# Performance work log

Hardware: AMD Instinct MI355X
Metric: run time of the kernel (lower is better)

## Reference

```python
import jax, jax.numpy as jnp
import numpy as np

H, W, K = 1024, 2048, 64


def _make_xy_coords(h, w):
    # matches torch buffer: xy_coords[0] = x coords (1..w), xy_coords[1] = y coords (1..h)
    x = jnp.tile(jnp.arange(1, w + 1, dtype=jnp.float32)[None, :], (h, 1))
    y = jnp.tile(jnp.arange(1, h + 1, dtype=jnp.float32)[:, None], (1, w))
    return jnp.stack((x, y), 0)  # (2, H, W)


def setup_inputs() -> dict:
    key = jax.random.key(0)
    k1, k2 = jax.random.split(key)
    instance_regressions = jax.random.normal(k1, (2, H, W), dtype=jnp.float32) * 32.0
    # center_coords[:, 0] = y in [0, H), center_coords[:, 1] = x in [0, W)
    u = jax.random.uniform(k2, (K, 2), dtype=jnp.float32)
    center_coords = u * jnp.array([H, W], dtype=jnp.float32)
    xy_coords = _make_xy_coords(H, W)
    return {
        "instance_regressions": instance_regressions,
        "center_coords": center_coords,
        "xy_coords": xy_coords,
    }


def reference(instance_regressions, center_coords, xy_coords):
    # predicted center for every pixel: (2, H, W)
    pred = xy_coords - instance_regressions
    px, py = pred[0], pred[1]                      # (H, W) each
    cy, cx = center_coords[:, 0], center_coords[:, 1]  # (k,) each; note column order
    dx = px[:, :, None] - cx[None, None, :]        # (H, W, k)
    dy = py[:, :, None] - cy[None, None, :]        # (H, W, k)
    dist = jnp.sqrt(dx * dx + dy * dy)             # (H, W, k)
    closest_inds = jnp.argmin(dist, axis=-1) + 1   # (H, W) int, 1-based instance ids
    return closest_inds
```

## Files before the change

### kernel.cpp

```cpp
#include <hip/hip_runtime.h>


#define H_ 1024
#define W_ 2048
#define K_ 64
#define TAU 8.0f

__global__ __launch_bounds__(256) void inst_map_kernel(
    const float* __restrict__ reg,
    const float* __restrict__ cc,
    int* __restrict__ out)
{
    __shared__ float4 cand[4][K_ + 1];

    const int tid  = threadIdx.x;
    const int w    = tid >> 6;
    const int lane = tid & 63;
    const int tr0  = blockIdx.y * 32;
    const int tc0  = blockIdx.x * 32;
    const int r    = tr0 + w * 8 + (lane >> 3);
    const int c    = tc0 + ((lane & 7) << 2);
    const int base = r * W_ + c;

    const float4 rx = *reinterpret_cast<const float4*>(reg + base);
    const float4 ry = *reinterpret_cast<const float4*>(reg + H_ * W_ + base);

    const float ax = (float)tc0 + 16.5f;
    const float ay = (float)(tr0 + w * 8) + 4.5f;

    float px[4], py[4];
    const float yf = (float)(r + 1);
    px[0] = (float)(c + 1) - rx.x;  py[0] = yf - ry.x;
    px[1] = (float)(c + 2) - rx.y;  py[1] = yf - ry.y;
    px[2] = (float)(c + 3) - rx.z;  py[2] = yf - ry.z;
    px[3] = (float)(c + 4) - rx.w;  py[3] = yf - ry.w;

    float pxn[4], pyn[4];
    float m = 0.0f;
    #pragma unroll
    for (int i = 0; i < 4; ++i) {
        const float sx = px[i] - ax, sy = py[i] - ay;
        pxn[i] = -2.0f * sx;
        pyn[i] = -2.0f * sy;
        m = fmaxf(m, sx * sx + sy * sy);
    }
    #pragma unroll
    for (int s = 1; s < 64; s <<= 1)
        m = fmaxf(m, __shfl_xor(m, s, 64));
    const float Rt = sqrtf(m);

    const float cyk = cc[2 * lane];
    const float cxk = cc[2 * lane + 1];
    const float sx = cxk - ax, sy = cyk - ay;
    const float ck = sx * sx + sy * sy;
    const float d  = sqrtf(ck);
    float dmin = d;
    #pragma unroll
    for (int s = 1; s < 64; s <<= 1)
        dmin = fminf(dmin, __shfl_xor(dmin, s, 64));
    const bool keep = d <= dmin + 2.0f * Rt + 4.0f;
    const unsigned long long mask = __ballot(keep);
    const int ncand = (int)__popcll(mask);
    if (keep) {
        const int pos = (int)__popcll(mask & ((1ull << lane) - 1ull));
        cand[w][pos] = make_float4(sx, sy, ck, __int_as_float(lane + 1));
    }
    if (lane == 0)
        cand[w][ncand] = make_float4(0.0f, 0.0f, INFINITY, __int_as_float(1));
    __syncthreads();

    float best[4] = {INFINITY, INFINITY, INFINITY, INFINITY};
    float sec[4]  = {INFINITY, INFINITY, INFINITY, INFINITY};
    int   bidx[4] = {1, 1, 1, 1};

    float4 cd = cand[w][0];
    for (int j = 0; j < ncand; ++j) {
        const float4 nx = cand[w][j + 1];
        #pragma unroll
        for (int i = 0; i < 4; ++i) {
            const float g = __fmaf_rn(pxn[i], cd.x,
                            __fmaf_rn(pyn[i], cd.y, cd.z));
            const bool lt = g < best[i];
            const float mn = fminf(sec[i], g);
            sec[i]  = lt ? best[i] : mn;
            best[i] = lt ? g : best[i];
            bidx[i] = lt ? __float_as_int(cd.w) : bidx[i];
        }
        cd = nx;
    }

    bool haz = false;
    #pragma unroll
    for (int i = 0; i < 4; ++i)
        haz = haz | (sec[i] - best[i] <= TAU);
    if (__any(haz)) {
        float sb[4]  = {INFINITY, INFINITY, INFINITY, INFINITY};
        int   bi2[4] = {1, 1, 1, 1};
        for (int j = 0; j < ncand; ++j) {
            const int kk = __float_as_int(cand[w][j].w);
            const float ecy = cc[2 * (kk - 1)];
            const float ecx = cc[2 * (kk - 1) + 1];
            #pragma unroll
            for (int i = 0; i < 4; ++i) {
                const float dx = px[i] - ecx;
                const float dy = py[i] - ecy;
                const float s2 = __fsqrt_rn(__fadd_rn(__fmul_rn(dx, dx),
                                                      __fmul_rn(dy, dy)));
                const bool lt = s2 < sb[i];
                sb[i]  = lt ? s2 : sb[i];
                bi2[i] = lt ? kk : bi2[i];
            }
        }
        #pragma unroll
        for (int i = 0; i < 4; ++i) bidx[i] = bi2[i];
    }

    *reinterpret_cast<int4*>(out + base) =
        make_int4(bidx[0], bidx[1], bidx[2], bidx[3]);
}

extern "C" void kernel_launch(void* const* d_in, const int* in_sizes, int n_in,
                              void* d_out, int out_size, void* d_ws, size_t ws_size,
                              hipStream_t stream) {
    const float* reg = (const float*)d_in[0];
    const float* cc  = (const float*)d_in[1];
    int* out = (int*)d_out;

    dim3 grid(W_ / 32, H_ / 32);
    inst_map_kernel<<<grid, 256, 0, stream>>>(reg, cc, out);
}
```

Measured before the change: 85.63 us.

## Process eight pixels per thread with wider tiles and nontemporal memory ops

Each thread now handles two rows of four pixels, so a block covers a 64x32 tile and the grid is halved. This amortises the per-wave candidate pruning, shuffles and barrier over twice as many pixels. Loads and stores become nontemporal, the two shuffle reductions are interleaved, and px/py are recomputed by reloading inputs only on the exact-fallback path to save registers. The hazard threshold TAU is raised to 16, which widens the fallback trigger, and the larger per-wave bounding radius keeps more candidates per wave.

```diff
diff --git a/kernel.cpp b/kernel.cpp
--- a/kernel.cpp
+++ b/kernel.cpp
@@ -4,7 +4,10 @@
 #define H_ 1024
 #define W_ 2048
 #define K_ 64
-#define TAU 8.0f
+#define TAU 16.0f
+
+typedef float  fx4 __attribute__((ext_vector_type(4)));
+typedef int    ix4 __attribute__((ext_vector_type(4)));
 
 __global__ __launch_bounds__(256) void inst_map_kernel(
     const float* __restrict__ reg,
@@ -17,67 +20,75 @@
     const int w    = tid >> 6;
     const int lane = tid & 63;
     const int tr0  = blockIdx.y * 32;
-    const int tc0  = blockIdx.x * 32;
-    const int r    = tr0 + w * 8 + (lane >> 3);
-    const int c    = tc0 + ((lane & 7) << 2);
-    const int base = r * W_ + c;
+    const int tc0  = blockIdx.x * 64;
+    const int r0    = tr0 + w * 8 + ((lane >> 4) << 1);
+    const int c     = tc0 + ((lane & 15) << 2);
+    const int base0 = r0 * W_ + c;
+    const int base1 = base0 + W_;
 
-    const float4 rx = *reinterpret_cast<const float4*>(reg + base);
-    const float4 ry = *reinterpret_cast<const float4*>(reg + H_ * W_ + base);
+    const fx4 rx0 = __builtin_nontemporal_load(
+        reinterpret_cast<const fx4*>(reg + base0));
+    const fx4 rx1 = __builtin_nontemporal_load(
+        reinterpret_cast<const fx4*>(reg + base1));
+    const fx4 ry0 = __builtin_nontemporal_load(
+        reinterpret_cast<const fx4*>(reg + H_ * W_ + base0));
+    const fx4 ry1 = __builtin_nontemporal_load(
+        reinterpret_cast<const fx4*>(reg + H_ * W_ + base1));
 
-    const float ax = (float)tc0 + 16.5f;
+    const float ax = (float)tc0 + 32.5f;
     const float ay = (float)(tr0 + w * 8) + 4.5f;
 
-    float px[4], py[4];
-    const float yf = (float)(r + 1);
-    px[0] = (float)(c + 1) - rx.x;  py[0] = yf - ry.x;
-    px[1] = (float)(c + 2) - rx.y;  py[1] = yf - ry.y;
-    px[2] = (float)(c + 3) - rx.z;  py[2] = yf - ry.z;
-    px[3] = (float)(c + 4) - rx.w;  py[3] = yf - ry.w;
-
-    float pxn[4], pyn[4];
+    float pxn[8], pyn[8];
     float m = 0.0f;
-    #pragma unroll
-    for (int i = 0; i < 4; ++i) {
-        const float sx = px[i] - ax, sy = py[i] - ay;
-        pxn[i] = -2.0f * sx;
-        pyn[i] = -2.0f * sy;
-        m = fmaxf(m, sx * sx + sy * sy);
+    {
+        const float rxv[8] = {rx0.x, rx0.y, rx0.z, rx0.w,
+                              rx1.x, rx1.y, rx1.z, rx1.w};
+        const float ryv[8] = {ry0.x, ry0.y, ry0.z, ry0.w,
+                              ry1.x, ry1.y, ry1.z, ry1.w};
+        #pragma unroll
+        for (int i = 0; i < 8; ++i) {
+            const float pxe = (float)(c + (i & 3) + 1) - rxv[i];
+            const float pye = (float)(r0 + (i >> 2) + 1) - ryv[i];
+            const float sx = pxe - ax, sy = pye - ay;
+            pxn[i] = -2.0f * sx;
+            pyn[i] = -2.0f * sy;
+            m = fmaxf(m, __fmaf_rn(sx, sx, sy * sy));
+        }
     }
-    #pragma unroll
-    for (int s = 1; s < 64; s <<= 1)
-        m = fmaxf(m, __shfl_xor(m, s, 64));
-    const float Rt = sqrtf(m);
 
     const float cyk = cc[2 * lane];
     const float cxk = cc[2 * lane + 1];
-    const float sx = cxk - ax, sy = cyk - ay;
-    const float ck = sx * sx + sy * sy;
-    const float d  = sqrtf(ck);
+    const float sxc = cxk - ax, syc = cyk - ay;
+    const float ck  = __fmaf_rn(sxc, sxc, syc * syc);
+    const float d   = sqrtf(ck);
     float dmin = d;
     #pragma unroll
-    for (int s = 1; s < 64; s <<= 1)
+    for (int s = 1; s < 64; s <<= 1) {
+        m    = fmaxf(m,    __shfl_xor(m, s, 64));
         dmin = fminf(dmin, __shfl_xor(dmin, s, 64));
-    const bool keep = d <= dmin + 2.0f * Rt + 4.0f;
+    }
+
+    const bool keep = d <= dmin + 2.0f * sqrtf(m) + 4.0f;
     const unsigned long long mask = __ballot(keep);
     const int ncand = (int)__popcll(mask);
     if (keep) {
         const int pos = (int)__popcll(mask & ((1ull << lane) - 1ull));
-        cand[w][pos] = make_float4(sx, sy, ck, __int_as_float(lane + 1));
+        cand[w][pos] = make_float4(sxc, syc, ck, __int_as_float(lane + 1));
     }
     if (lane == 0)
         cand[w][ncand] = make_float4(0.0f, 0.0f, INFINITY, __int_as_float(1));
     __syncthreads();
 
-    float best[4] = {INFINITY, INFINITY, INFINITY, INFINITY};
-    float sec[4]  = {INFINITY, INFINITY, INFINITY, INFINITY};
-    int   bidx[4] = {1, 1, 1, 1};
+    float best[8], sec[8];
+    int   bidx[8];
+    #pragma unroll
+    for (int i = 0; i < 8; ++i) { best[i] = INFINITY; sec[i] = INFINITY; bidx[i] = 1; }
 
     float4 cd = cand[w][0];
     for (int j = 0; j < ncand; ++j) {
         const float4 nx = cand[w][j + 1];
         #pragma unroll
-        for (int i = 0; i < 4; ++i) {
+        for (int i = 0; i < 8; ++i) {
             const float g = __fmaf_rn(pxn[i], cd.x,
                             __fmaf_rn(pyn[i], cd.y, cd.z));
             const bool lt = g < best[i];
@@ -91,17 +102,32 @@
 
     bool haz = false;
     #pragma unroll
-    for (int i = 0; i < 4; ++i)
+    for (int i = 0; i < 8; ++i)
         haz = haz | (sec[i] - best[i] <= TAU);
     if (__any(haz)) {
-        float sb[4]  = {INFINITY, INFINITY, INFINITY, INFINITY};
-        int   bi2[4] = {1, 1, 1, 1};
+        const float4 ex0 = *reinterpret_cast<const float4*>(reg + base0);
+        const float4 ex1 = *reinterpret_cast<const float4*>(reg + base1);
+        const float4 ey0 = *reinterpret_cast<const float4*>(reg + H_ * W_ + base0);
+        const float4 ey1 = *reinterpret_cast<const float4*>(reg + H_ * W_ + base1);
+        const float rxv[8] = {ex0.x, ex0.y, ex0.z, ex0.w,
+                              ex1.x, ex1.y, ex1.z, ex1.w};
+        const float ryv[8] = {ey0.x, ey0.y, ey0.z, ey0.w,
+                              ey1.x, ey1.y, ey1.z, ey1.w};
+        float px[8], py[8], sb[8];
+        int bi2[8];
+        #pragma unroll
+        for (int i = 0; i < 8; ++i) {
+            px[i] = (float)(c + (i & 3) + 1) - rxv[i];
+            py[i] = (float)(r0 + (i >> 2) + 1) - ryv[i];
+            sb[i] = INFINITY;
+            bi2[i] = 1;
+        }
         for (int j = 0; j < ncand; ++j) {
             const int kk = __float_as_int(cand[w][j].w);
             const float ecy = cc[2 * (kk - 1)];
             const float ecx = cc[2 * (kk - 1) + 1];
             #pragma unroll
-            for (int i = 0; i < 4; ++i) {
+            for (int i = 0; i < 8; ++i) {
                 const float dx = px[i] - ecx;
                 const float dy = py[i] - ecy;
                 const float s2 = __fsqrt_rn(__fadd_rn(__fmul_rn(dx, dx),
@@ -112,11 +138,13 @@
             }
         }
         #pragma unroll
-        for (int i = 0; i < 4; ++i) bidx[i] = bi2[i];
+        for (int i = 0; i < 8; ++i) bidx[i] = bi2[i];
     }
 
-    *reinterpret_cast<int4*>(out + base) =
-        make_int4(bidx[0], bidx[1], bidx[2], bidx[3]);
+    const ix4 o0 = {bidx[0], bidx[1], bidx[2], bidx[3]};
+    const ix4 o1 = {bidx[4], bidx[5], bidx[6], bidx[7]};
+    __builtin_nontemporal_store(o0, reinterpret_cast<ix4*>(out + base0));
+    __builtin_nontemporal_store(o1, reinterpret_cast<ix4*>(out + base1));
 }
 
 extern "C" void kernel_launch(void* const* d_in, const int* in_sizes, int n_in,
@@ -126,6 +154,6 @@
     const float* cc  = (const float*)d_in[1];
     int* out = (int*)d_out;
 
-    dim3 grid(W_ / 32, H_ / 32);
+    dim3 grid(W_ / 64, H_ / 32);
     inst_map_kernel<<<grid, 256, 0, stream>>>(reg, cc, out);
 }
```

After: 92.89 us. 1.08x slower.

## Compute exact squared distances with relative hazard check, drop syncthreads, nontemporal store

Applied to the files above, without the earlier changes.

The candidate scan now computes the true squared distance per candidate instead of the expanded dot-product form with a fixed absolute gap threshold. A near-tie is flagged only when a new minimum lies within a tiny relative margin of the previous best, so the exact sqrt fallback should fire much less often. The two wave reductions are interleaved into one loop, the block-wide __syncthreads is removed because each wave reads only its own shared slot, and the output uses a nontemporal vector store. The per-candidate inner loop does somewhat more arithmetic, and the hazard check only compares against the running best, so ties with later non-winning candidates are not flagged.

```diff
diff --git a/kernel.cpp b/kernel.cpp
--- a/kernel.cpp
+++ b/kernel.cpp
@@ -4,7 +4,9 @@
 #define H_ 1024
 #define W_ 2048
 #define K_ 64
-#define TAU 8.0f
+#define HAZC 1.9073486e-6f
+
+typedef int ix4 __attribute__((ext_vector_type(4)));
 
 __global__ __launch_bounds__(256) void inst_map_kernel(
     const float* __restrict__ reg,
@@ -25,9 +27,6 @@
     const float4 rx = *reinterpret_cast<const float4*>(reg + base);
     const float4 ry = *reinterpret_cast<const float4*>(reg + H_ * W_ + base);
 
-    const float ax = (float)tc0 + 16.5f;
-    const float ay = (float)(tr0 + w * 8) + 4.5f;
-
     float px[4], py[4];
     const float yf = (float)(r + 1);
     px[0] = (float)(c + 1) - rx.x;  py[0] = yf - ry.x;
@@ -35,69 +34,62 @@
     px[2] = (float)(c + 3) - rx.z;  py[2] = yf - ry.z;
     px[3] = (float)(c + 4) - rx.w;  py[3] = yf - ry.w;
 
-    float pxn[4], pyn[4];
+    const float ax = (float)tc0 + 16.5f;
+    const float ay = (float)(tr0 + w * 8) + 4.5f;
     float m = 0.0f;
     #pragma unroll
     for (int i = 0; i < 4; ++i) {
         const float sx = px[i] - ax, sy = py[i] - ay;
-        pxn[i] = -2.0f * sx;
-        pyn[i] = -2.0f * sy;
-        m = fmaxf(m, sx * sx + sy * sy);
+        m = fmaxf(m, __fmaf_rn(sx, sx, sy * sy));
     }
-    #pragma unroll
-    for (int s = 1; s < 64; s <<= 1)
-        m = fmaxf(m, __shfl_xor(m, s, 64));
-    const float Rt = sqrtf(m);
 
     const float cyk = cc[2 * lane];
     const float cxk = cc[2 * lane + 1];
-    const float sx = cxk - ax, sy = cyk - ay;
-    const float ck = sx * sx + sy * sy;
-    const float d  = sqrtf(ck);
+    const float sxc = cxk - ax, syc = cyk - ay;
+    const float d   = sqrtf(__fmaf_rn(sxc, sxc, syc * syc));
     float dmin = d;
     #pragma unroll
-    for (int s = 1; s < 64; s <<= 1)
+    for (int s = 1; s < 64; s <<= 1) {
+        m    = fmaxf(m,    __shfl_xor(m, s, 64));
         dmin = fminf(dmin, __shfl_xor(dmin, s, 64));
-    const bool keep = d <= dmin + 2.0f * Rt + 4.0f;
+    }
+
+    const bool keep = d <= dmin + 2.0f * sqrtf(m) + 4.0f;
     const unsigned long long mask = __ballot(keep);
     const int ncand = (int)__popcll(mask);
     if (keep) {
         const int pos = (int)__popcll(mask & ((1ull << lane) - 1ull));
-        cand[w][pos] = make_float4(sx, sy, ck, __int_as_float(lane + 1));
+        cand[w][pos] = make_float4(cxk, cyk, __int_as_float(lane + 1), 0.0f);
     }
     if (lane == 0)
-        cand[w][ncand] = make_float4(0.0f, 0.0f, INFINITY, __int_as_float(1));
-    __syncthreads();
+        cand[w][ncand] = make_float4(INFINITY, INFINITY, __int_as_float(1), 0.0f);
 
     float best[4] = {INFINITY, INFINITY, INFINITY, INFINITY};
-    float sec[4]  = {INFINITY, INFINITY, INFINITY, INFINITY};
     int   bidx[4] = {1, 1, 1, 1};
+    bool  haz = false;
 
     float4 cd = cand[w][0];
     for (int j = 0; j < ncand; ++j) {
         const float4 nx = cand[w][j + 1];
         #pragma unroll
         for (int i = 0; i < 4; ++i) {
-            const float g = __fmaf_rn(pxn[i], cd.x,
-                            __fmaf_rn(pyn[i], cd.y, cd.z));
-            const bool lt = g < best[i];
-            const float mn = fminf(sec[i], g);
-            sec[i]  = lt ? best[i] : mn;
-            best[i] = lt ? g : best[i];
-            bidx[i] = lt ? __float_as_int(cd.w) : bidx[i];
+            const float dx = px[i] - cd.x;
+            const float dy = py[i] - cd.y;
+            const float d2 = __fadd_rn(__fmul_rn(dx, dx), __fmul_rn(dy, dy));
+            const bool lt = d2 < best[i];
+            haz = haz | (lt & (best[i] - d2 <= __fmul_rn(d2, HAZC)));
+            best[i] = lt ? d2 : best[i];
+            bidx[i] = lt ? __float_as_int(cd.z) : bidx[i];
         }
         cd = nx;
     }
 
-    bool haz = false;
-    #pragma unroll
-    for (int i = 0; i < 4; ++i)
-        haz = haz | (sec[i] - best[i] <= TAU);
     if (__any(haz)) {
         float sb[4]  = {INFINITY, INFINITY, INFINITY, INFINITY};
         int   bi2[4] = {1, 1, 1, 1};
         for (int j = 0; j < ncand; ++j) {
-            const int kk = __float_as_int(cand[w][j].w);
+            const float4 c2 = cand[w][j];
+            const int kk = __float_as_int(c2.z);
             const float ecy = cc[2 * (kk - 1)];
             const float ecx = cc[2 * (kk - 1) + 1];
             #pragma unroll
@@ -115,8 +107,8 @@
         for (int i = 0; i < 4; ++i) bidx[i] = bi2[i];
     }
 
-    *reinterpret_cast<int4*>(out + base) =
-        make_int4(bidx[0], bidx[1], bidx[2], bidx[3]);
+    const ix4 o = {bidx[0], bidx[1], bidx[2], bidx[3]};
+    __builtin_nontemporal_store(o, reinterpret_cast<ix4*>(out + base));
 }
 
 extern "C" void kernel_launch(void* const* d_in, const int* in_sizes, int n_in,
```

Result: faster. 82.02 us, median of 2 (-4.2%).

## Drop block barrier, adaptive hazard threshold, fused shuffles, nontemporal output stores

Applied to the files above, without the earlier changes.

Removes the __syncthreads, since each wave only reads its own candidate list in shared memory. Interleaves the max and min shuffle reductions, and replaces the fixed tie threshold with a relative-plus-absolute bound so fewer waves fall into the exact fallback. The fallback now reloads the regression values instead of keeping px/py live, which cuts register pressure. Output is written with nontemporal stores. The risk is a cross-lane shared-memory ordering issue within the wave once the barrier is gone, and the new threshold has to stay conservative for correctness.

```diff
diff --git a/kernel.cpp b/kernel.cpp
--- a/kernel.cpp
+++ b/kernel.cpp
@@ -4,7 +4,10 @@
 #define H_ 1024
 #define W_ 2048
 #define K_ 64
-#define TAU 8.0f
+#define RELW 9.5367431640625e-7f
+#define ABSW 4.0f
+
+typedef int ix4 __attribute__((ext_vector_type(4)));
 
 __global__ __launch_bounds__(256) void inst_map_kernel(
     const float* __restrict__ reg,
@@ -28,46 +31,44 @@
     const float ax = (float)tc0 + 16.5f;
     const float ay = (float)(tr0 + w * 8) + 4.5f;
 
-    float px[4], py[4];
-    const float yf = (float)(r + 1);
-    px[0] = (float)(c + 1) - rx.x;  py[0] = yf - ry.x;
-    px[1] = (float)(c + 2) - rx.y;  py[1] = yf - ry.y;
-    px[2] = (float)(c + 3) - rx.z;  py[2] = yf - ry.z;
-    px[3] = (float)(c + 4) - rx.w;  py[3] = yf - ry.w;
-
-    float pxn[4], pyn[4];
-    float m = 0.0f;
-    #pragma unroll
-    for (int i = 0; i < 4; ++i) {
-        const float sx = px[i] - ax, sy = py[i] - ay;
-        pxn[i] = -2.0f * sx;
-        pyn[i] = -2.0f * sy;
-        m = fmaxf(m, sx * sx + sy * sy);
+    float pxn[4], pyn[4], h[4];
+    {
+        const float cshift = (float)c - ax;
+        const float rshift = (float)(r + 1) - ay;
+        const float rv[4] = {rx.x, rx.y, rx.z, rx.w};
+        const float yv[4] = {ry.x, ry.y, ry.z, ry.w};
+        #pragma unroll
+        for (int i = 0; i < 4; ++i) {
+            const float sx = (cshift + (float)(i + 1)) - rv[i];
+            const float sy = rshift - yv[i];
+            pxn[i] = -2.0f * sx;
+            pyn[i] = -2.0f * sy;
+            h[i]   = __fmaf_rn(sx, sx, sy * sy);
+        }
     }
-    #pragma unroll
-    for (int s = 1; s < 64; s <<= 1)
-        m = fmaxf(m, __shfl_xor(m, s, 64));
-    const float Rt = sqrtf(m);
+    float m = fmaxf(fmaxf(h[0], h[1]), fmaxf(h[2], h[3]));
 
     const float cyk = cc[2 * lane];
     const float cxk = cc[2 * lane + 1];
-    const float sx = cxk - ax, sy = cyk - ay;
-    const float ck = sx * sx + sy * sy;
-    const float d  = sqrtf(ck);
+    const float sxc = cxk - ax, syc = cyk - ay;
+    const float ck  = __fmaf_rn(sxc, sxc, syc * syc);
+    const float d   = sqrtf(ck);
     float dmin = d;
     #pragma unroll
-    for (int s = 1; s < 64; s <<= 1)
+    for (int s = 1; s < 64; s <<= 1) {
+        m    = fmaxf(m,    __shfl_xor(m, s, 64));
         dmin = fminf(dmin, __shfl_xor(dmin, s, 64));
-    const bool keep = d <= dmin + 2.0f * Rt + 4.0f;
+    }
+
+    const bool keep = d <= dmin + 2.0f * sqrtf(m) + 4.0f;
     const unsigned long long mask = __ballot(keep);
     const int ncand = (int)__popcll(mask);
     if (keep) {
         const int pos = (int)__popcll(mask & ((1ull << lane) - 1ull));
-        cand[w][pos] = make_float4(sx, sy, ck, __int_as_float(lane + 1));
+        cand[w][pos] = make_float4(sxc, syc, ck, __int_as_float(lane + 1));
     }
     if (lane == 0)
         cand[w][ncand] = make_float4(0.0f, 0.0f, INFINITY, __int_as_float(1));
-    __syncthreads();
 
     float best[4] = {INFINITY, INFINITY, INFINITY, INFINITY};
     float sec[4]  = {INFINITY, INFINITY, INFINITY, INFINITY};
@@ -92,10 +93,24 @@
     bool haz = false;
     #pragma unroll
     for (int i = 0; i < 4; ++i)
-        haz = haz | (sec[i] - best[i] <= TAU);
+        haz = haz | (sec[i] - best[i] <=
+                     __fmaf_rn(best[i] + h[i], RELW, ABSW));
+
     if (__any(haz)) {
-        float sb[4]  = {INFINITY, INFINITY, INFINITY, INFINITY};
-        int   bi2[4] = {1, 1, 1, 1};
+        const float4 ex = *reinterpret_cast<const float4*>(reg + base);
+        const float4 ey = *reinterpret_cast<const float4*>(reg + H_ * W_ + base);
+        const float rv[4] = {ex.x, ex.y, ex.z, ex.w};
+        const float yv[4] = {ey.x, ey.y, ey.z, ey.w};
+        float px[4], py[4], sb[4];
+        int bi2[4];
+        const float yf = (float)(r + 1);
+        #pragma unroll
+        for (int i = 0; i < 4; ++i) {
+            px[i] = (float)(c + i + 1) - rv[i];
+            py[i] = yf - yv[i];
+            sb[i] = INFINITY;
+            bi2[i] = 1;
+        }
         for (int j = 0; j < ncand; ++j) {
             const int kk = __float_as_int(cand[w][j].w);
             const float ecy = cc[2 * (kk - 1)];
@@ -115,8 +130,8 @@
         for (int i = 0; i < 4; ++i) bidx[i] = bi2[i];
     }
 
-    *reinterpret_cast<int4*>(out + base) =
-        make_int4(bidx[0], bidx[1], bidx[2], bidx[3]);
+    const ix4 o = {bidx[0], bidx[1], bidx[2], bidx[3]};
+    __builtin_nontemporal_store(o, reinterpret_cast<ix4*>(out + base));
 }
 
 extern "C" void kernel_launch(void* const* d_in, const int* in_sizes, int n_in,
```

Result: faster. 83.75 us (-2.2%).
